# Performance work log

Hardware: AMD Instinct MI355X
Metric: run time of the kernel (lower is better)

## Reference

```python
import jax, jax.numpy as jnp
import numpy as np

B, S, D, H, CLIP = 4, 1024, 1024, 16, 64
DH = D // H

def setup_inputs() -> dict:
    key = jax.random.key(0)
    ks = jax.random.split(key, 10)
    sc = 1.0 / np.sqrt(D)
    return {
        "queries": jax.random.normal(ks[0], (B, S, D), jnp.float32),
        "keys": jax.random.normal(ks[1], (B, S, D), jnp.float32),
        "values": jax.random.normal(ks[2], (B, S, D), jnp.float32),
        "valid_lens": jax.random.randint(ks[3], (B,), 0, S),
        "Wq": jax.random.normal(ks[4], (D, D), jnp.float32) * sc,
        "Wk": jax.random.normal(ks[5], (D, D), jnp.float32) * sc,
        "Wv": jax.random.normal(ks[6], (D, D), jnp.float32) * sc,
        "Wo": jax.random.normal(ks[7], (D, D), jnp.float32) * sc,
        "rpr_k": jax.random.normal(ks[8], (2 * CLIP + 1, DH), jnp.float32),
        "rpr_v": jax.random.normal(ks[9], (2 * CLIP + 1, DH), jnp.float32),
    }

def reference(queries, keys, values, valid_lens, Wq, Wk, Wv, Wo, rpr_k, rpr_v):
    # project and split heads: [B,S,D] -> [B,H,S,DH]
    def split(x, W):
        return (x @ W).reshape(B, S, H, DH).transpose(0, 2, 1, 3)
    q = split(queries, Wq)
    k = split(keys, Wk)
    v = split(values, Wv)
    # relative position indices [S,S] in [0, 2*CLIP]
    dist = jnp.arange(S)[None, :] - jnp.arange(S)[:, None]
    dist = jnp.clip(dist, -CLIP, CLIP) + CLIP
    pos_k = rpr_k[dist]  # [S,S,DH]
    pos_v = rpr_v[dist]  # [S,S,DH]
    # content scores + relative-position key bias
    scores = jnp.einsum('bhqd,bhkd->bhqk', q, k)
    scores = scores + jnp.einsum('bhqd,qkd->bhqk', q, pos_k)
    scores = scores / jnp.sqrt(jnp.asarray(DH, q.dtype))
    # masked softmax: positions >= valid_len set to -1e6 (matches torch code)
    key_mask = jnp.arange(S)[None, None, None, :] < valid_lens[:, None, None, None]
    scores = jnp.where(key_mask, scores, jnp.asarray(-1e6, scores.dtype))
    attn = jax.nn.softmax(scores, axis=-1)  # [B,H,S,S]
    # value aggregation + relative-position value bias
    out = jnp.einsum('bhqk,bhkd->bhqd', attn, v)
    out = out + jnp.einsum('bhqk,qkd->bhqd', attn, pos_v)
    out = out.transpose(0, 2, 1, 3).reshape(B, S, D)
    return out @ Wo
```

## Files before the change

### kernel.cpp

```cpp
#include <hip/hip_runtime.h>
#include <stdint.h>
#include <math.h>

#define BB 4
#define SS 1024
#define DD 1024
#define HH 16
#define DHH 64
#define NCLIP 64
#define NCC 129
#define NCP 160
#define QRSTR 148
#define M0F 20.0f

typedef __bf16 bf16;
typedef __bf16 bf16x8 __attribute__((ext_vector_type(8)));
typedef float f32x4 __attribute__((ext_vector_type(4)));

__device__ __forceinline__ void gload_lds16(const void* g, void* l) {
  __builtin_amdgcn_global_load_lds((const __attribute__((address_space(1))) void*)g,
                                   (__attribute__((address_space(3))) void*)l, 16, 0, 0);
}

struct TpArgs { const float* w[4]; bf16* wt[4]; };
__global__ __launch_bounds__(256) void transpose_pack_w(TpArgs args) {
  const float* __restrict__ W = args.w[blockIdx.z];
  bf16* __restrict__ Wt = args.wt[blockIdx.z];
  __shared__ float tile[32][33];
  int tx = threadIdx.x, ty = threadIdx.y;
  int n0 = blockIdx.x * 32, k0 = blockIdx.y * 32;
#pragma unroll
  for (int i = 0; i < 4; i++)
    tile[ty + i * 8][tx] = W[(size_t)(k0 + ty + i * 8) * DD + n0 + tx];
  __syncthreads();
#pragma unroll
  for (int i = 0; i < 4; i++)
    Wt[(size_t)(n0 + ty + i * 8) * DD + k0 + tx] = (bf16)tile[tx][ty + i * 8];
}

struct CvtArgs { const float* in[3]; bf16* out[3]; int skip[3]; };
__global__ __launch_bounds__(256) void f32_to_bf16_3(CvtArgs args, const int* __restrict__ vlens) {
  const int z = blockIdx.z;
  if (args.skip[z]) {
    int row0 = (blockIdx.x * 2) & 1023;
    int b = (blockIdx.x * 2) >> 10;
    int vl = vlens[b];
    if (vl > 0 && row0 >= vl) return;
  }
  const float* __restrict__ in = args.in[z];
  bf16* __restrict__ out = args.out[z];
  size_t i = ((size_t)blockIdx.x * 256 + threadIdx.x) * 8;
  f32x4 v0 = *(const f32x4*)(in + i);
  f32x4 v1 = *(const f32x4*)(in + i + 4);
  bf16x8 o;
#pragma unroll
  for (int j = 0; j < 4; j++) { o[j] = (bf16)v0[j]; o[j + 4] = (bf16)v1[j]; }
  *(bf16x8*)(out + i) = o;
}

struct GemmArgs { const bf16* a[3]; const bf16* bt[3]; void* c[3]; float sc[3]; int skip[3]; };
template <bool SPLIT>
__global__ __launch_bounds__(256) void gemm128(GemmArgs args, const int* __restrict__ vlens) {
  const int z = blockIdx.z;
  const int m0 = blockIdx.y * 128, n0 = blockIdx.x * 128;
  if (args.skip[z]) {
    int vl = vlens[m0 >> 10];
    if (vl > 0 && (m0 & 1023) >= vl) return;
  }
  const bf16* __restrict__ A  = args.a[z];
  const bf16* __restrict__ Bt = args.bt[z];
  void* __restrict__ Cv = args.c[z];
  const float scale = args.sc[z];
  __shared__ __align__(16) bf16 As[128][32];
  __shared__ __align__(16) bf16 Bs[128][32];
  const int tid = threadIdx.x, lane = tid & 63, wv = tid >> 6;
  const int wr = wv >> 1, wc = wv & 1;
  const int l15 = lane & 15, l4 = lane >> 4;
  const int srow = lane >> 2, scol = (lane & 3) * 8;
  f32x4 z4 = {0.f, 0.f, 0.f, 0.f};
  f32x4 acc[4][4];
#pragma unroll
  for (int i = 0; i < 4; i++)
#pragma unroll
    for (int j = 0; j < 4; j++) acc[i][j] = z4;

  for (int k0 = 0; k0 < DD; k0 += 32) {
    gload_lds16(A  + (size_t)(m0 + wv * 16 + srow) * DD + k0 + scol,      &As[wv * 16][0]);
    gload_lds16(A  + (size_t)(m0 + 64 + wv * 16 + srow) * DD + k0 + scol, &As[64 + wv * 16][0]);
    gload_lds16(Bt + (size_t)(n0 + wv * 16 + srow) * DD + k0 + scol,      &Bs[wv * 16][0]);
    gload_lds16(Bt + (size_t)(n0 + 64 + wv * 16 + srow) * DD + k0 + scol, &Bs[64 + wv * 16][0]);
    __syncthreads();
    bf16x8 af[4], bfv[4];
#pragma unroll
    for (int i = 0; i < 4; i++) {
      af[i]  = *(const bf16x8*)&As[wr * 64 + i * 16 + l15][l4 * 8];
      bfv[i] = *(const bf16x8*)&Bs[wc * 64 + i * 16 + l15][l4 * 8];
    }
#pragma unroll
    for (int mi = 0; mi < 4; mi++)
#pragma unroll
      for (int ni = 0; ni < 4; ni++)
        acc[mi][ni] = __builtin_amdgcn_mfma_f32_16x16x32_bf16(af[mi], bfv[ni], acc[mi][ni], 0, 0, 0);
    __syncthreads();
  }
#pragma unroll
  for (int mi = 0; mi < 4; mi++)
#pragma unroll
    for (int ni = 0; ni < 4; ni++)
#pragma unroll
      for (int r = 0; r < 4; r++) {
        int m = m0 + wr * 64 + mi * 16 + l4 * 4 + r;
        int n = n0 + wc * 64 + ni * 16 + l15;
        float val = acc[mi][ni][r] * scale;
        if (SPLIT) {
          ((bf16*)Cv)[((((size_t)(m >> 10) * HH + (n >> 6)) * SS) + (m & 1023)) * DHH + (n & 63)] =
              (bf16)val;
        } else {
          ((float*)Cv)[(size_t)m * DD + n] = val;
        }
      }
}

__global__ __launch_bounds__(256) void gemm_bf16_final(const bf16* __restrict__ A,
                                                       const bf16* __restrict__ Bt,
                                                       float* __restrict__ C) {
  __shared__ __align__(16) bf16 As[64][32];
  __shared__ __align__(16) bf16 Bs[128][32];
  const int tid = threadIdx.x, lane = tid & 63, wv = tid >> 6;
  const int l15 = lane & 15, l4 = lane >> 4;
  const int m0 = blockIdx.y * 64, n0 = blockIdx.x * 128;
  const int srow = lane >> 2, scol = (lane & 3) * 8;
  f32x4 z4 = {0.f, 0.f, 0.f, 0.f};
  f32x4 acc[4][2];
#pragma unroll
  for (int i = 0; i < 4; i++) { acc[i][0] = z4; acc[i][1] = z4; }

  for (int k0 = 0; k0 < DD; k0 += 32) {
    gload_lds16(A + (size_t)(m0 + wv * 16 + srow) * DD + k0 + scol, &As[wv * 16][0]);
    gload_lds16(Bt + (size_t)(n0 + wv * 32 + srow) * DD + k0 + scol, &Bs[wv * 32][0]);
    gload_lds16(Bt + (size_t)(n0 + wv * 32 + 16 + srow) * DD + k0 + scol, &Bs[wv * 32 + 16][0]);
    __syncthreads();
    bf16x8 af[4], bfv[2];
#pragma unroll
    for (int i = 0; i < 4; i++) af[i] = *(const bf16x8*)&As[i * 16 + l15][l4 * 8];
#pragma unroll
    for (int i = 0; i < 2; i++) bfv[i] = *(const bf16x8*)&Bs[wv * 32 + i * 16 + l15][l4 * 8];
#pragma unroll
    for (int mi = 0; mi < 4; mi++)
#pragma unroll
      for (int ni = 0; ni < 2; ni++)
        acc[mi][ni] = __builtin_amdgcn_mfma_f32_16x16x32_bf16(af[mi], bfv[ni], acc[mi][ni], 0, 0, 0);
    __syncthreads();
  }
#pragma unroll
  for (int mi = 0; mi < 4; mi++)
#pragma unroll
    for (int ni = 0; ni < 2; ni++)
#pragma unroll
      for (int r = 0; r < 4; r++) {
        int m = m0 + mi * 16 + l4 * 4 + r;
        int n = n0 + wv * 32 + ni * 16 + l15;
        C[(size_t)m * DD + n] = acc[mi][ni][r];
      }
}

__global__ __launch_bounds__(256) void vh_transpose(const bf16* __restrict__ Vh,
                                                    bf16* __restrict__ VhT,
                                                    const int* __restrict__ vlens) {
  __shared__ bf16 til[64][65];
  int bh = blockIdx.y;
  int s0 = blockIdx.x * 64;
  int vl = vlens[bh >> 4];
  if (vl > 0 && s0 >= vl + 32) return;
  const bf16* src = Vh + (size_t)bh * SS * DHH + (size_t)s0 * DHH;
  for (int i = threadIdx.x; i < 64 * 64; i += 256) {
    int r = i >> 6, cc = i & 63;
    til[r][cc] = src[(size_t)r * DHH + cc];
  }
  __syncthreads();
  bf16* dst = VhT + (size_t)bh * DHH * SS + s0;
  for (int i = threadIdx.x; i < 64 * 64; i += 256) {
    int d = i >> 6, cc = i & 63;
    dst[(size_t)d * SS + cc] = til[cc][d];
  }
}

__global__ void prep_tables(const float* __restrict__ rpr_v, const float* __restrict__ rpr_k,
                            bf16* __restrict__ rvT, bf16* __restrict__ rkP) {
  int i = blockIdx.x * 256 + threadIdx.x;
  if (i < DHH * NCP) {
    int d = i / NCP, c = i - d * NCP;
    rvT[i] = (c < NCC) ? (bf16)rpr_v[(size_t)c * DHH + d] : (bf16)0.f;
  }
  if (i < 144 * 64) {
    rkP[i] = (i < NCC * DHH) ? (bf16)rpr_k[i] : (bf16)0.f;
  }
}

__global__ __launch_bounds__(256, 3) void attn_mfma(
    const bf16* __restrict__ Qh, const bf16* __restrict__ Kh, const bf16* __restrict__ VhT,
    const bf16* __restrict__ rkP, const int* __restrict__ valid_lens,
    const bf16* __restrict__ rvT, bf16* __restrict__ Obh) {
  __shared__ __align__(16) bf16 Ks[2][32][64];
  __shared__ __align__(16) char arena[4][10240];
  const int tid = threadIdx.x, lane = tid & 63, w = tid >> 6;
  const int l15 = lane & 15, l4 = lane >> 4;
  const int b = blockIdx.z, h = blockIdx.y, bh = b * HH + h;
  const int q0 = blockIdx.x * 64 + w * 16;
  const int vlen = valid_lens[b];
  const float mval = (vlen == 0) ? 0.f : -30000.f;
  char* base = arena[w];
  bf16* QRs = (bf16*)base;
  _Float16* SBand = (_Float16*)(base + 4736);
  bf16* Pl = (bf16*)(base + 8832);

  const bf16* Qbase = Qh + ((size_t)bh * SS + q0) * DHH;
  bf16x8 qa0 = *(const bf16x8*)(Qbase + (size_t)l15 * DHH + l4 * 8);
  bf16x8 qa1 = *(const bf16x8*)(Qbase + (size_t)l15 * DHH + 32 + l4 * 8);
  const bf16* Kbase = Kh + (size_t)bh * SS * DHH;
  const bf16* Vbase = VhT + (size_t)bh * DHH * SS;
  f32x4 z = {0.f, 0.f, 0.f, 0.f};

#pragma unroll
  for (int ni = 0; ni < 9; ni++) {
    const bf16* rp = rkP + (size_t)(ni * 16 + l15) * DHH + l4 * 8;
    bf16x8 b0 = *(const bf16x8*)(rp);
    bf16x8 b1 = *(const bf16x8*)(rp + 32);
    f32x4 acc = __builtin_amdgcn_mfma_f32_16x16x32_bf16(qa0, b0, z, 0, 0, 0);
    acc = __builtin_amdgcn_mfma_f32_16x16x32_bf16(qa1, b1, acc, 0, 0, 0);
#pragma unroll
    for (int r = 0; r < 4; r++)
      QRs[(l4 * 4 + r) * QRSTR + ni * 16 + l15] = (bf16)acc[r];
  }
  {
    _Float16 ninf = (_Float16)(-65504.f);
    for (int i = lane; i < 16 * 128; i += 64) SBand[i] = ninf;
  }

  float biasLo[4], biasHi[4];
#pragma unroll
  for (int r = 0; r < 4; r++) {
    biasLo[r] = (float)QRs[(l4 * 4 + r) * QRSTR + 0];
    biasHi[r] = (float)QRs[(l4 * 4 + r) * QRSTR + 128];
  }

  float l_lane[4], slo[4], shi[4];
#pragma unroll
  for (int r = 0; r < 4; r++) { l_lane[r] = 0.f; slo[r] = 0.f; shi[r] = 0.f; }
  f32x4 acco[4];
#pragma unroll
  for (int i = 0; i < 4; i++) acco[i] = z;

  const int krow = w * 8 + (lane >> 3);
  const int kch  = ((lane & 7) ^ (krow & 7)) * 8;
  const int ksw0 = (l4 ^ (l15 & 7)) * 8;
  const int ksw1 = ((l4 + 4) ^ (l15 & 7)) * 8;

  const int kfb = (vlen > 0) ? (vlen & ~31) : 0;
  const int kte = (vlen > 0) ? ((vlen + 31) & ~31) : SS;
  int bs = q0 - 94; bs = (bs < 0) ? 0 : ((bs + 31) & ~31);
  int be = (q0 + 110) & ~31; if (be > SS) be = SS;

  gload_lds16(Kbase + (size_t)krow * DHH + kch, &Ks[0][w * 8][0]);
  __syncthreads();

  int cur = 0;
  for (int ks = 0; ks < kte; ks += 32) {
    if (ks + 32 < kte)
      gload_lds16(Kbase + (size_t)(ks + 32 + krow) * DHH + kch, &Ks[cur ^ 1][w * 8][0]);

    bf16x8 kf00 = *(const bf16x8*)&Ks[cur][l15][ksw0];
    bf16x8 kf01 = *(const bf16x8*)&Ks[cur][l15][ksw1];
    bf16x8 kf10 = *(const bf16x8*)&Ks[cur][16 + l15][ksw0];
    bf16x8 kf11 = *(const bf16x8*)&Ks[cur][16 + l15][ksw1];
    f32x4 a0 = __builtin_amdgcn_mfma_f32_16x16x32_bf16(qa0, kf00, z, 0, 0, 0);
    a0 = __builtin_amdgcn_mfma_f32_16x16x32_bf16(qa1, kf01, a0, 0, 0, 0);
    f32x4 a1 = __builtin_amdgcn_mfma_f32_16x16x32_bf16(qa0, kf10, z, 0, 0, 0);
    a1 = __builtin_amdgcn_mfma_f32_16x16x32_bf16(qa1, kf11, a1, 0, 0, 0);

    if (ks >= kfb) {
      const int rel = ks - q0;
      const int mode = (rel <= -95) ? 0 : (rel >= 79) ? 1 : 2;
#pragma unroll
      for (int sub = 0; sub < 2; sub++) {
        const f32x4 a = sub ? a1 : a0;
        const int kg = ks + sub * 16 + l15;
        const bool msk = (kg >= vlen);
        if (mode == 0) {
#pragma unroll
          for (int r = 0; r < 4; r++) {
            float s = msk ? mval : (a[r] + biasLo[r]);
            float p = __expf(s - M0F);
            l_lane[r] += p; slo[r] += p;
            Pl[(l4 * 4 + r) * 40 + sub * 16 + l15] = (bf16)p;
          }
        } else if (mode == 1) {
#pragma unroll
          for (int r = 0; r < 4; r++) {
            float s = msk ? mval : (a[r] + biasHi[r]);
            float p = __expf(s - M0F);
            l_lane[r] += p; shi[r] += p;
            Pl[(l4 * 4 + r) * 40 + sub * 16 + l15] = (bf16)p;
          }
        } else {
#pragma unroll
          for (int r = 0; r < 4; r++) {
            const int qloc = l4 * 4 + r;
            int dlt = kg - q0 - qloc;
            int c = (dlt < -NCLIP ? -NCLIP : (dlt > NCLIP ? NCLIP : dlt)) + NCLIP;
            float s = a[r] + (float)QRs[qloc * QRSTR + c];
            if (msk) s = mval;
            if (dlt > -64 && dlt < 64) SBand[qloc * 128 + dlt + 63] = (_Float16)s;
            float p = __expf(s - M0F);
            l_lane[r] += p;
            slo[r] += (dlt <= -64) ? p : 0.f;
            shi[r] += (dlt >= 64) ? p : 0.f;
            Pl[qloc * 40 + sub * 16 + l15] = (bf16)p;
          }
        }
      }
    } else if (ks < bs) {
#pragma unroll
      for (int sub = 0; sub < 2; sub++) {
        const f32x4 a = sub ? a1 : a0;
#pragma unroll
        for (int r = 0; r < 4; r++) {
          float p = __expf(a[r] + biasLo[r] - M0F);
          l_lane[r] += p; slo[r] += p;
          Pl[(l4 * 4 + r) * 40 + sub * 16 + l15] = (bf16)p;
        }
      }
    } else if (ks < be) {
#pragma unroll
      for (int sub = 0; sub < 2; sub++) {
        const f32x4 a = sub ? a1 : a0;
        const int kg = ks + sub * 16 + l15;
#pragma unroll
        for (int r = 0; r < 4; r++) {
          const int qloc = l4 * 4 + r;
          int dlt = kg - q0 - qloc;
          int c = (dlt < -NCLIP ? -NCLIP : (dlt > NCLIP ? NCLIP : dlt)) + NCLIP;
          float s = a[r] + (float)QRs[qloc * QRSTR + c];
          if (dlt > -64 && dlt < 64) SBand[qloc * 128 + dlt + 63] = (_Float16)s;
          float p = __expf(s - M0F);
          l_lane[r] += p;
          slo[r] += (dlt <= -64) ? p : 0.f;
          shi[r] += (dlt >= 64) ? p : 0.f;
          Pl[qloc * 40 + sub * 16 + l15] = (bf16)p;
        }
      }
    } else {
#pragma unroll
      for (int sub = 0; sub < 2; sub++) {
        const f32x4 a = sub ? a1 : a0;
#pragma unroll
        for (int r = 0; r < 4; r++) {
          float p = __expf(a[r] + biasHi[r] - M0F);
          l_lane[r] += p; shi[r] += p;
          Pl[(l4 * 4 + r) * 40 + sub * 16 + l15] = (bf16)p;
        }
      }
    }

    bf16x8 pa = *(const bf16x8*)&Pl[l15 * 40 + l4 * 8];
    const bf16* vp = Vbase + (size_t)l15 * SS + ks + l4 * 8;
    acco[0] = __builtin_amdgcn_mfma_f32_16x16x32_bf16(pa, *(const bf16x8*)(vp), acco[0], 0, 0, 0);
    acco[1] = __builtin_amdgcn_mfma_f32_16x16x32_bf16(pa, *(const bf16x8*)(vp + (size_t)16 * SS), acco[1], 0, 0, 0);
    acco[2] = __builtin_amdgcn_mfma_f32_16x16x32_bf16(pa, *(const bf16x8*)(vp + (size_t)32 * SS), acco[2], 0, 0, 0);
    acco[3] = __builtin_amdgcn_mfma_f32_16x16x32_bf16(pa, *(const bf16x8*)(vp + (size_t)48 * SS), acco[3], 0, 0, 0);
    __syncthreads();
    cur ^= 1;
  }

  float* li_s   = (float*)(base + 8832);
  float* a0_s   = (float*)(base + 8896);
  float* a128_s = (float*)(base + 8960);
  float li_r[4];
#pragma unroll
  for (int r = 0; r < 4; r++) {
    const int qloc = l4 * 4 + r;
    float lt = l_lane[r], so = slo[r], sh = shi[r];
    lt += __shfl_xor(lt, 1, 64); so += __shfl_xor(so, 1, 64); sh += __shfl_xor(sh, 1, 64);
    lt += __shfl_xor(lt, 2, 64); so += __shfl_xor(so, 2, 64); sh += __shfl_xor(sh, 2, 64);
    lt += __shfl_xor(lt, 4, 64); so += __shfl_xor(so, 4, 64); sh += __shfl_xor(sh, 4, 64);
    lt += __shfl_xor(lt, 8, 64); so += __shfl_xor(so, 8, 64); sh += __shfl_xor(sh, 8, 64);
    float li = 1.f / lt;
    li_r[r] = li;
    if (l15 == 0) { li_s[qloc] = li; a0_s[qloc] = so * li; a128_s[qloc] = sh * li; }
  }
  bf16* AWs = (bf16*)base;
  for (int row = 0; row < 16; row++) {
    float li = li_s[row], a0 = a0_s[row], a128 = a128_s[row];
#pragma unroll
    for (int j = 0; j < 3; j++) {
      int c = lane + 64 * j;
      if (c < 160) {
        float val;
        if (c == 0) val = a0;
        else if (c == 128) val = a128;
        else if (c < 128) val = __expf((float)SBand[row * 128 + c - 1] - M0F) * li;
        else val = 0.f;
        AWs[row * 168 + c] = (bf16)val;
      }
    }
  }
  f32x4 acc2[4];
#pragma unroll
  for (int i = 0; i < 4; i++) acc2[i] = z;
#pragma unroll
  for (int kk = 0; kk < 5; kk++) {
    bf16x8 af = *(const bf16x8*)&AWs[l15 * 168 + kk * 32 + l4 * 8];
#pragma unroll
    for (int ni = 0; ni < 4; ni++) {
      bf16x8 bv = *(const bf16x8*)(rvT + (size_t)(ni * 16 + l15) * NCP + kk * 32 + l4 * 8);
      acc2[ni] = __builtin_amdgcn_mfma_f32_16x16x32_bf16(af, bv, acc2[ni], 0, 0, 0);
    }
  }
#pragma unroll
  for (int ni = 0; ni < 4; ni++)
#pragma unroll
    for (int r = 0; r < 4; r++) {
      int qg = q0 + l4 * 4 + r;
      Obh[((size_t)b * SS + qg) * DD + h * DHH + ni * 16 + l15] =
          (bf16)(acco[ni][r] * li_r[r] + acc2[ni][r]);
    }
}

extern "C" void kernel_launch(void* const* d_in, const int* in_sizes, int n_in,
                              void* d_out, int out_size, void* d_ws, size_t ws_size,
                              hipStream_t stream) {
  (void)in_sizes; (void)n_in; (void)out_size; (void)ws_size;
  const float* queries = (const float*)d_in[0];
  const float* keys    = (const float*)d_in[1];
  const float* values  = (const float*)d_in[2];
  const int*   vlens   = (const int*)d_in[3];
  const float* Wq = (const float*)d_in[4];
  const float* Wk = (const float*)d_in[5];
  const float* Wv = (const float*)d_in[6];
  const float* Wo = (const float*)d_in[7];
  const float* rpr_k = (const float*)d_in[8];
  const float* rpr_v = (const float*)d_in[9];

  char* ws = (char*)d_ws;
  const size_t MB = 1024 * 1024;
  bf16* Wtq  = (bf16*)(ws + 0 * MB);
  bf16* Wtk  = (bf16*)(ws + 2 * MB);
  bf16* Wtv  = (bf16*)(ws + 4 * MB);
  bf16* Wto  = (bf16*)(ws + 6 * MB);
  bf16* Qh   = (bf16*)(ws + 8 * MB);
  bf16* Kh   = (bf16*)(ws + 16 * MB);
  bf16* Vh   = (bf16*)(ws + 24 * MB);
  bf16* VhT  = (bf16*)(ws + 32 * MB);
  bf16* Qb   = (bf16*)(ws + 40 * MB);
  bf16* Kb   = (bf16*)(ws + 48 * MB);
  bf16* Vb   = (bf16*)(ws + 56 * MB);
  bf16* Obh  = (bf16*)(ws + 64 * MB);
  bf16* rvT  = (bf16*)(ws + 72 * MB);
  bf16* rkP  = (bf16*)(ws + 73 * MB);

  TpArgs tp; tp.w[0] = Wq; tp.w[1] = Wk; tp.w[2] = Wv; tp.w[3] = Wo;
  tp.wt[0] = Wtq; tp.wt[1] = Wtk; tp.wt[2] = Wtv; tp.wt[3] = Wto;
  transpose_pack_w<<<dim3(32, 32, 4), dim3(32, 8), 0, stream>>>(tp);

  CvtArgs cv; cv.in[0] = queries; cv.in[1] = keys; cv.in[2] = values;
  cv.out[0] = Qb; cv.out[1] = Kb; cv.out[2] = Vb;
  cv.skip[0] = 0; cv.skip[1] = 1; cv.skip[2] = 1;
  f32_to_bf16_3<<<dim3(2048, 1, 3), 256, 0, stream>>>(cv, vlens);

  GemmArgs gp;
  gp.a[0] = Qb; gp.a[1] = Kb; gp.a[2] = Vb;
  gp.bt[0] = Wtq; gp.bt[1] = Wtk; gp.bt[2] = Wtv;
  gp.c[0] = (void*)Qh; gp.c[1] = (void*)Kh; gp.c[2] = (void*)Vh;
  gp.sc[0] = 0.125f; gp.sc[1] = 1.0f; gp.sc[2] = 1.0f;
  gp.skip[0] = 0; gp.skip[1] = 1; gp.skip[2] = 1;
  gemm128<true><<<dim3(8, 32, 3), 256, 0, stream>>>(gp, vlens);

  vh_transpose<<<dim3(16, 64), 256, 0, stream>>>(Vh, VhT, vlens);
  prep_tables<<<dim3(40), 256, 0, stream>>>(rpr_v, rpr_k, rvT, rkP);
  attn_mfma<<<dim3(16, HH, BB), 256, 0, stream>>>(Qh, Kh, VhT, rkP, vlens, rvT, Obh);
  gemm_bf16_final<<<dim3(8, 64), 256, 0, stream>>>(Obh, Wto, (float*)d_out);
}
```

Baseline: 120.1 us.

## Widen attention key tile to 64 and drop LDS double buffering

The attention kernel now processes 64 keys per iteration instead of 32. It computes four QK MFMA sub-tiles and two PV MFMA steps per tile, and widens the P staging stride to 72. The double-buffered K prefetch is replaced by a single 64-row LDS tile loaded at the top of each iteration and guarded by a barrier. This halves the number of loop iterations and barriers, but it gives up the overlap between loading the next K tile and computing on the current one. Band and tail boundaries, the per-warp arena size and the V-transpose early-exit bound change to match the new tile size, and more work past valid_len may be done when it is rounded up to 64.

```diff
diff --git a/kernel.cpp b/kernel.cpp
--- a/kernel.cpp
+++ b/kernel.cpp
@@ -171,7 +171,7 @@
   int bh = blockIdx.y;
   int s0 = blockIdx.x * 64;
   int vl = vlens[bh >> 4];
-  if (vl > 0 && s0 >= vl + 32) return;
+  if (vl > 0 && s0 >= vl + 64) return;
   const bf16* src = Vh + (size_t)bh * SS * DHH + (size_t)s0 * DHH;
   for (int i = threadIdx.x; i < 64 * 64; i += 256) {
     int r = i >> 6, cc = i & 63;
@@ -201,8 +201,8 @@
     const bf16* __restrict__ Qh, const bf16* __restrict__ Kh, const bf16* __restrict__ VhT,
     const bf16* __restrict__ rkP, const int* __restrict__ valid_lens,
     const bf16* __restrict__ rvT, bf16* __restrict__ Obh) {
-  __shared__ __align__(16) bf16 Ks[2][32][64];
-  __shared__ __align__(16) char arena[4][10240];
+  __shared__ __align__(16) bf16 Ks[64][64];
+  __shared__ __align__(16) char arena[4][11264];
   const int tid = threadIdx.x, lane = tid & 63, w = tid >> 6;
   const int l15 = lane & 15, l4 = lane >> 4;
   const int b = blockIdx.z, h = blockIdx.y, bh = b * HH + h;
@@ -251,39 +251,35 @@
 #pragma unroll
   for (int i = 0; i < 4; i++) acco[i] = z;
 
-  const int krow = w * 8 + (lane >> 3);
+  const int krow = w * 16 + (lane >> 3);
   const int kch  = ((lane & 7) ^ (krow & 7)) * 8;
   const int ksw0 = (l4 ^ (l15 & 7)) * 8;
   const int ksw1 = ((l4 + 4) ^ (l15 & 7)) * 8;
 
-  const int kfb = (vlen > 0) ? (vlen & ~31) : 0;
-  const int kte = (vlen > 0) ? ((vlen + 31) & ~31) : SS;
-  int bs = q0 - 94; bs = (bs < 0) ? 0 : ((bs + 31) & ~31);
-  int be = (q0 + 110) & ~31; if (be > SS) be = SS;
-
-  gload_lds16(Kbase + (size_t)krow * DHH + kch, &Ks[0][w * 8][0]);
-  __syncthreads();
-
-  int cur = 0;
-  for (int ks = 0; ks < kte; ks += 32) {
-    if (ks + 32 < kte)
-      gload_lds16(Kbase + (size_t)(ks + 32 + krow) * DHH + kch, &Ks[cur ^ 1][w * 8][0]);
-
-    bf16x8 kf00 = *(const bf16x8*)&Ks[cur][l15][ksw0];
-    bf16x8 kf01 = *(const bf16x8*)&Ks[cur][l15][ksw1];
-    bf16x8 kf10 = *(const bf16x8*)&Ks[cur][16 + l15][ksw0];
-    bf16x8 kf11 = *(const bf16x8*)&Ks[cur][16 + l15][ksw1];
-    f32x4 a0 = __builtin_amdgcn_mfma_f32_16x16x32_bf16(qa0, kf00, z, 0, 0, 0);
-    a0 = __builtin_amdgcn_mfma_f32_16x16x32_bf16(qa1, kf01, a0, 0, 0, 0);
-    f32x4 a1 = __builtin_amdgcn_mfma_f32_16x16x32_bf16(qa0, kf10, z, 0, 0, 0);
-    a1 = __builtin_amdgcn_mfma_f32_16x16x32_bf16(qa1, kf11, a1, 0, 0, 0);
+  const int kfb = (vlen > 0) ? (vlen & ~63) : 0;
+  const int kte = (vlen > 0) ? ((vlen + 63) & ~63) : SS;
+  int bs = q0 - 126; bs = (bs < 0) ? 0 : ((bs + 63) & ~63);
+  int be = (q0 + 79 + 63) & ~63; if (be > SS) be = SS;
+
+  for (int ks = 0; ks < kte; ks += 64) {
+    gload_lds16(Kbase + (size_t)(ks + krow) * DHH + kch, &Ks[w * 16][0]);
+    gload_lds16(Kbase + (size_t)(ks + krow + 8) * DHH + kch, &Ks[w * 16 + 8][0]);
+    __syncthreads();
+    f32x4 aa[4];
+#pragma unroll
+    for (int sub = 0; sub < 4; sub++) {
+      bf16x8 kf0 = *(const bf16x8*)&Ks[sub * 16 + l15][ksw0];
+      bf16x8 kf1 = *(const bf16x8*)&Ks[sub * 16 + l15][ksw1];
+      f32x4 a = __builtin_amdgcn_mfma_f32_16x16x32_bf16(qa0, kf0, z, 0, 0, 0);
+      aa[sub] = __builtin_amdgcn_mfma_f32_16x16x32_bf16(qa1, kf1, a, 0, 0, 0);
+    }
 
     if (ks >= kfb) {
       const int rel = ks - q0;
-      const int mode = (rel <= -95) ? 0 : (rel >= 79) ? 1 : 2;
-#pragma unroll
-      for (int sub = 0; sub < 2; sub++) {
-        const f32x4 a = sub ? a1 : a0;
+      const int mode = (rel <= -127) ? 0 : (rel >= 79) ? 1 : 2;
+#pragma unroll
+      for (int sub = 0; sub < 4; sub++) {
+        const f32x4 a = aa[sub];
         const int kg = ks + sub * 16 + l15;
         const bool msk = (kg >= vlen);
         if (mode == 0) {
@@ -292,7 +288,7 @@
             float s = msk ? mval : (a[r] + biasLo[r]);
             float p = __expf(s - M0F);
             l_lane[r] += p; slo[r] += p;
-            Pl[(l4 * 4 + r) * 40 + sub * 16 + l15] = (bf16)p;
+            Pl[(l4 * 4 + r) * 72 + sub * 16 + l15] = (bf16)p;
           }
         } else if (mode == 1) {
 #pragma unroll
@@ -300,7 +296,7 @@
             float s = msk ? mval : (a[r] + biasHi[r]);
             float p = __expf(s - M0F);
             l_lane[r] += p; shi[r] += p;
-            Pl[(l4 * 4 + r) * 40 + sub * 16 + l15] = (bf16)p;
+            Pl[(l4 * 4 + r) * 72 + sub * 16 + l15] = (bf16)p;
           }
         } else {
 #pragma unroll
@@ -315,25 +311,25 @@
             l_lane[r] += p;
             slo[r] += (dlt <= -64) ? p : 0.f;
             shi[r] += (dlt >= 64) ? p : 0.f;
-            Pl[qloc * 40 + sub * 16 + l15] = (bf16)p;
+            Pl[qloc * 72 + sub * 16 + l15] = (bf16)p;
           }
         }
       }
     } else if (ks < bs) {
 #pragma unroll
-      for (int sub = 0; sub < 2; sub++) {
-        const f32x4 a = sub ? a1 : a0;
+      for (int sub = 0; sub < 4; sub++) {
+        const f32x4 a = aa[sub];
 #pragma unroll
         for (int r = 0; r < 4; r++) {
           float p = __expf(a[r] + biasLo[r] - M0F);
           l_lane[r] += p; slo[r] += p;
-          Pl[(l4 * 4 + r) * 40 + sub * 16 + l15] = (bf16)p;
+          Pl[(l4 * 4 + r) * 72 + sub * 16 + l15] = (bf16)p;
         }
       }
     } else if (ks < be) {
 #pragma unroll
-      for (int sub = 0; sub < 2; sub++) {
-        const f32x4 a = sub ? a1 : a0;
+      for (int sub = 0; sub < 4; sub++) {
+        const f32x4 a = aa[sub];
         const int kg = ks + sub * 16 + l15;
 #pragma unroll
         for (int r = 0; r < 4; r++) {
@@ -346,30 +342,31 @@
           l_lane[r] += p;
           slo[r] += (dlt <= -64) ? p : 0.f;
           shi[r] += (dlt >= 64) ? p : 0.f;
-          Pl[qloc * 40 + sub * 16 + l15] = (bf16)p;
+          Pl[qloc * 72 + sub * 16 + l15] = (bf16)p;
         }
       }
     } else {
 #pragma unroll
-      for (int sub = 0; sub < 2; sub++) {
-        const f32x4 a = sub ? a1 : a0;
+      for (int sub = 0; sub < 4; sub++) {
+        const f32x4 a = aa[sub];
 #pragma unroll
         for (int r = 0; r < 4; r++) {
           float p = __expf(a[r] + biasHi[r] - M0F);
           l_lane[r] += p; shi[r] += p;
-          Pl[(l4 * 4 + r) * 40 + sub * 16 + l15] = (bf16)p;
+          Pl[(l4 * 4 + r) * 72 + sub * 16 + l15] = (bf16)p;
         }
       }
     }
 
-    bf16x8 pa = *(const bf16x8*)&Pl[l15 * 40 + l4 * 8];
-    const bf16* vp = Vbase + (size_t)l15 * SS + ks + l4 * 8;
-    acco[0] = __builtin_amdgcn_mfma_f32_16x16x32_bf16(pa, *(const bf16x8*)(vp), acco[0], 0, 0, 0);
-    acco[1] = __builtin_amdgcn_mfma_f32_16x16x32_bf16(pa, *(const bf16x8*)(vp + (size_t)16 * SS), acco[1], 0, 0, 0);
-    acco[2] = __builtin_amdgcn_mfma_f32_16x16x32_bf16(pa, *(const bf16x8*)(vp + (size_t)32 * SS), acco[2], 0, 0, 0);
-    acco[3] = __builtin_amdgcn_mfma_f32_16x16x32_bf16(pa, *(const bf16x8*)(vp + (size_t)48 * SS), acco[3], 0, 0, 0);
-    __syncthreads();
-    cur ^= 1;
+    bf16x8 pa0 = *(const bf16x8*)&Pl[l15 * 72 + l4 * 8];
+    bf16x8 pa1 = *(const bf16x8*)&Pl[l15 * 72 + 32 + l4 * 8];
+#pragma unroll
+    for (int ni = 0; ni < 4; ni++) {
+      const bf16* vp = Vbase + (size_t)(ni * 16 + l15) * SS + ks + l4 * 8;
+      acco[ni] = __builtin_amdgcn_mfma_f32_16x16x32_bf16(pa0, *(const bf16x8*)(vp), acco[ni], 0, 0, 0);
+      acco[ni] = __builtin_amdgcn_mfma_f32_16x16x32_bf16(pa1, *(const bf16x8*)(vp + 32), acco[ni], 0, 0, 0);
+    }
+    __syncthreads();
   }
 
   float* li_s   = (float*)(base + 8832);
```

After: 123.9 us. +3.1%, slower.
